# Performance work log

Measured on AMD Instinct MI355X. Metric: run time of the kernel, lower is better.

The kernel has to match this reference:

```python
import jax, jax.numpy as jnp
import numpy as np

N = 100000
E = 3200000
FEAT_DIMS = [512, 256, 128]
NUM_GNN = 2
NUM_MLP = 2
EPS = 1e-12


def l2norm(x):
    # F.normalize(x, dim=1, p=2)
    n = jnp.sqrt(jnp.sum(x * x, axis=1, keepdims=True))
    return x / jnp.maximum(n, EPS)


def setup_inputs() -> dict:
    key = jax.random.key(0)
    ks = jax.random.split(key, 16)
    D = FEAT_DIMS[-1]
    inp = {
        "feat": jax.random.normal(ks[0], (N, FEAT_DIMS[0]), dtype=jnp.float32),
        "sup_rows": jax.random.randint(ks[1], (E,), 0, N, dtype=jnp.int32),
        "sup_cols": jax.random.randint(ks[2], (E,), 0, N, dtype=jnp.int32),
        "sup_vals": jax.random.uniform(ks[3], (E,), dtype=jnp.float32),
        # feature-reduction linears (stored [in, out])
        "W_feat0": jax.random.normal(ks[4], (FEAT_DIMS[0], FEAT_DIMS[1]), dtype=jnp.float32) * 0.05,
        "b_feat0": jnp.zeros((FEAT_DIMS[1],), dtype=jnp.float32),
        "W_feat1": jax.random.normal(ks[5], (FEAT_DIMS[1], FEAT_DIMS[2]), dtype=jnp.float32) * 0.05,
        "b_feat1": jnp.zeros((FEAT_DIMS[2],), dtype=jnp.float32),
        # GCN layers (bias=False)
        "W_gnn": jax.random.normal(ks[6], (NUM_GNN, D, D), dtype=jnp.float32) * 0.05,
        # final emb linear map
        "W_emb": jax.random.normal(ks[7], (D, D), dtype=jnp.float32) * 0.05,
        "b_emb": jnp.zeros((D,), dtype=jnp.float32),
        # temperature MLP towers
        "W_lft": jax.random.normal(ks[8], (NUM_MLP, D, D), dtype=jnp.float32) * 0.05,
        "b_lft": jnp.zeros((NUM_MLP, D), dtype=jnp.float32),
        "W_rgt": jax.random.normal(ks[9], (NUM_MLP, D, D), dtype=jnp.float32) * 0.05,
        "b_rgt": jnp.zeros((NUM_MLP, D), dtype=jnp.float32),
    }
    return inp


def _forward(feat, sup_rows, sup_cols, sup_vals,
             W_feat0, b_feat0, W_feat1, b_feat1,
             W_gnn, W_emb, b_emb, W_lft, b_lft, W_rgt, b_rgt):
    # non-linear feature reduction (dropout = identity in eval mode)
    x = jnp.tanh(feat @ W_feat0 + b_feat0)
    x = jnp.tanh(x @ W_feat1 + b_feat1)

    def spmm(emb):
        # sparse support @ emb via gather + segment-sum
        msgs = sup_vals[:, None] * emb[sup_cols]           # [E, D]
        return jax.ops.segment_sum(msgs, sup_rows, num_segments=N)

    gnn_in = x
    gnn_acc = x
    gnn_out = x
    for l in range(NUM_GNN):
        h = spmm(gnn_in)
        h = jnp.tanh(h @ W_gnn[l])
        gnn_out = l2norm(h)
        gnn_in = gnn_out
        gnn_acc = gnn_acc + gnn_out

    emb = l2norm(gnn_acc @ W_emb + b_emb)

    lft_in = gnn_out
    rgt_in = gnn_out
    for l in range(NUM_MLP):
        lft = jnp.tanh(lft_in @ W_lft[l] + b_lft[l])
        rgt = jnp.tanh(rgt_in @ W_rgt[l] + b_rgt[l])
        if l < NUM_MLP - 1:
            lft = lft + lft_in
            rgt = rgt + rgt_in
        lft_in, rgt_in = lft, rgt
    return emb, lft_in, rgt_in


def reference(feat, sup_rows, sup_cols, sup_vals,
              W_feat0, b_feat0, W_feat1, b_feat1,
              W_gnn, W_emb, b_emb, W_lft, b_lft, W_rgt, b_rgt):
    return _forward(feat, sup_rows, sup_cols, sup_vals,
                    W_feat0, b_feat0, W_feat1, b_feat1,
                    W_gnn, W_emb, b_emb, W_lft, b_lft, W_rgt, b_rgt)
```

## Files before the change

kernel.cpp:

```cpp
#include <hip/hip_runtime.h>
#include <math.h>

typedef short bf16x8 __attribute__((ext_vector_type(8)));
typedef float f32x4  __attribute__((ext_vector_type(4)));

__device__ __forceinline__ unsigned short f2bf(float x) {
    unsigned u = __float_as_uint(x);
    unsigned r = u + 0x7FFFu + ((u >> 16) & 1u);
    return (unsigned short)(r >> 16);
}
__device__ __forceinline__ float bf2f(unsigned short b) {
    return __uint_as_float(((unsigned)b) << 16);
}

__global__ __launch_bounds__(256)
void wconvD(const float* __restrict__ W, unsigned short* __restrict__ Wt, int K, int N)
{
    int id = blockIdx.x * 256 + threadIdx.x;
    if (id >= K * N) return;
    int c = id / K, k = id - c * K;
    int kblk = k >> 5, ksub = (k >> 3) & 3, kel = k & 7;
    int cblk = c >> 6, n = c & 3, lr = (c >> 2) & 15;
    int lane = lr + (ksub << 4);
    size_t dst = ((((size_t)kblk * (N >> 6) + cblk) * 4 + n) << 9) + (lane << 3) + kel;
    Wt[dst] = f2bf(W[(size_t)k * N + c]);
}

__global__ __launch_bounds__(256)
void wconv7(const float* __restrict__ Wg, const float* __restrict__ Wemb,
            const float* __restrict__ Wl, const float* __restrict__ Wr,
            unsigned short* __restrict__ dst)
{
    int id = blockIdx.x * 256 + threadIdx.x;
    if (id >= 7 * 16384) return;
    int m = id >> 14, r = id & 16383;
    int c = r >> 7, k = r & 127;
    const float* src = (m < 2) ? (Wg + m * 16384)
                     : (m == 2) ? Wemb
                     : (m < 5) ? (Wl + (m - 3) * 16384)
                               : (Wr + (m - 5) * 16384);
    int n = c & 7, lr = (c >> 3) & 15;
    int ks = k >> 5, ksub = (k >> 3) & 3, kel = k & 7;
    int lane = lr + (ksub << 4);
    dst[(size_t)m * 16384 + (((ks << 3) + n) << 9) + (lane << 3) + kel] = f2bf(src[(size_t)k * 128 + c]);
}

__global__ __launch_bounds__(256)
void f32_to_bf16(const float* __restrict__ in, unsigned short* __restrict__ outb, long n8)
{
    long id = (long)blockIdx.x * 256 + threadIdx.x;
    if (id >= n8) return;
    const float4* p = (const float4*)(in + id * 8);
    float4 a = p[0], b = p[1];
    *(ushort4*)(outb + id * 8)     = make_ushort4(f2bf(a.x), f2bf(a.y), f2bf(a.z), f2bf(a.w));
    *(ushort4*)(outb + id * 8 + 4) = make_ushort4(f2bf(b.x), f2bf(b.y), f2bf(b.z), f2bf(b.w));
}

__global__ __launch_bounds__(256)
void mfma_direct(const unsigned short* __restrict__ Ab, const unsigned short* __restrict__ Wt,
                 const float* __restrict__ bias, unsigned short* __restrict__ out_bf,
                 int M, int K, int Ncols)
{
    const int tid  = threadIdx.x;
    const int row0 = blockIdx.x * 128;
    const int col0 = blockIdx.y * 128;
    const int wv   = tid >> 6, lane = tid & 63;
    const int wr   = (wv >> 1) * 64, wc = (wv & 1) * 64;
    const int lr   = lane & 15;
    const int lk8  = (lane >> 4) * 8;
    const int ncb  = Ncols >> 6;
    const int cp   = (col0 + wc) >> 6;

    const unsigned short* arow[4];
#pragma unroll
    for (int m = 0; m < 4; m++) {
        int r = row0 + wr + m * 16 + lr;
        r = r < M ? r : (M - 1);
        arow[m] = Ab + (size_t)r * K + lk8;
    }
    const unsigned short* bb = Wt + (((size_t)cp * 4) << 9) + (lane << 3);
    const size_t bstep = (size_t)ncb * 2048;

    f32x4 acc[4][4];
#pragma unroll
    for (int m = 0; m < 4; m++)
#pragma unroll
        for (int n = 0; n < 4; n++)
#pragma unroll
            for (int j = 0; j < 4; j++) acc[m][n][j] = 0.f;

#pragma unroll 2
    for (int kk = 0; kk < K; kk += 32) {
        bf16x8 af[4], bfr[4];
#pragma unroll
        for (int m = 0; m < 4; m++) af[m]  = *(const bf16x8*)(arow[m] + kk);
        const unsigned short* bk = bb + (size_t)(kk >> 5) * bstep;
#pragma unroll
        for (int n = 0; n < 4; n++) bfr[n] = *(const bf16x8*)(bk + (n << 9));
#pragma unroll
        for (int m = 0; m < 4; m++)
#pragma unroll
            for (int n = 0; n < 4; n++)
                acc[m][n] = __builtin_amdgcn_mfma_f32_16x16x32_bf16(af[m], bfr[n], acc[m][n], 0, 0, 0);
    }

    const int cbase = col0 + wc + lr * 4;
    float4 b4 = *(const float4*)(bias + cbase);
    float bv[4] = {b4.x, b4.y, b4.z, b4.w};
    const int rbase = (lane >> 4) * 4;
#pragma unroll
    for (int m = 0; m < 4; m++) {
#pragma unroll
        for (int j = 0; j < 4; j++) {
            int row = row0 + wr + m * 16 + rbase + j;
            if (row < M) {
                ushort4 o;
                o.x = f2bf(tanhf(acc[m][0][j] + bv[0]));
                o.y = f2bf(tanhf(acc[m][1][j] + bv[1]));
                o.z = f2bf(tanhf(acc[m][2][j] + bv[2]));
                o.w = f2bf(tanhf(acc[m][3][j] + bv[3]));
                *(ushort4*)(out_bf + (size_t)row * Ncols + cbase) = o;
            }
        }
    }
}

template<bool ABF16, bool TANH, bool L2, bool RESID, bool AUX, bool AUXBF,
         bool F32OUT, bool BF16OUT, bool BIAS>
__global__ __launch_bounds__(256)
void mfma_ep(const void* __restrict__ A_, const unsigned short* __restrict__ Wt,
             const float* __restrict__ bias, const unsigned short* __restrict__ resid_bf,
             const void* __restrict__ aux_in, float* __restrict__ aux_out,
             float* __restrict__ out, unsigned short* __restrict__ out_bf, int M)
{
    const int tid  = threadIdx.x;
    const int row0 = blockIdx.x * 64;
    const int wv   = tid >> 6, lane = tid & 63;
    const int lr   = lane & 15;
    const int lk8  = (lane >> 4) * 8;
    const int wr   = wv * 16;

    const unsigned short* Abr;
    const float*          Afr;
    {
        int r = row0 + wr + lr;
        r = r < M ? r : (M - 1);
        Abr = (const unsigned short*)A_ + ((size_t)r << 7) + lk8;
        Afr = (const float*)A_          + ((size_t)r << 7) + lk8;
    }
    const unsigned short* wb = Wt + (lane << 3);

    f32x4 acc[8];
#pragma unroll
    for (int n = 0; n < 8; n++)
#pragma unroll
        for (int j = 0; j < 4; j++) acc[n][j] = 0.f;

#pragma unroll 2
    for (int ks = 0; ks < 4; ks++) {
        bf16x8 af, bn[8];
        if (ABF16) af = *(const bf16x8*)(Abr + ks * 32);
        else {
            float4 a = *(const float4*)(Afr + ks * 32);
            float4 b = *(const float4*)(Afr + ks * 32 + 4);
            af[0]=(short)f2bf(a.x); af[1]=(short)f2bf(a.y); af[2]=(short)f2bf(a.z); af[3]=(short)f2bf(a.w);
            af[4]=(short)f2bf(b.x); af[5]=(short)f2bf(b.y); af[6]=(short)f2bf(b.z); af[7]=(short)f2bf(b.w);
        }
#pragma unroll
        for (int n = 0; n < 8; n++)
            bn[n] = *(const bf16x8*)(wb + ((((ks << 3) + n)) << 9));
#pragma unroll
        for (int n = 0; n < 8; n++)
            acc[n] = __builtin_amdgcn_mfma_f32_16x16x32_bf16(af, bn[n], acc[n], 0, 0, 0);
    }

    const int cbase = lr * 8;
    float bv[8];
    if (BIAS) {
        float4 b0 = *(const float4*)(bias + cbase);
        float4 b1 = *(const float4*)(bias + cbase + 4);
        bv[0]=b0.x; bv[1]=b0.y; bv[2]=b0.z; bv[3]=b0.w;
        bv[4]=b1.x; bv[5]=b1.y; bv[6]=b1.z; bv[7]=b1.w;
    } else {
#pragma unroll
        for (int n = 0; n < 8; n++) bv[n] = 0.f;
    }
    const int rbase = (lane >> 4) * 4;

#pragma unroll
    for (int j = 0; j < 4; j++) {
        int row = row0 + wr + rbase + j;
        bool ok = row < M;
        size_t base = ((size_t)row << 7) + cbase;
        float v[8];
#pragma unroll
        for (int n = 0; n < 8; n++) {
            v[n] = acc[n][j] + bv[n];
            if (TANH) v[n] = tanhf(v[n]);
        }
        if (RESID) {
            if (ok) {
                bf16x8 rv = *(const bf16x8*)(resid_bf + base);
#pragma unroll
                for (int n = 0; n < 8; n++) v[n] += bf2f((unsigned short)rv[n]);
            }
        }
        if (L2) {
            float s = 0.f;
#pragma unroll
            for (int n = 0; n < 8; n++) s += v[n] * v[n];
#pragma unroll
            for (int msk = 8; msk >= 1; msk >>= 1) s += __shfl_xor(s, msk);
            float sc = 1.f / fmaxf(sqrtf(s), 1e-12f);
#pragma unroll
            for (int n = 0; n < 8; n++) v[n] *= sc;
        }
        if (ok) {
            if (F32OUT) {
                *(float4*)(out + base)     = make_float4(v[0], v[1], v[2], v[3]);
                *(float4*)(out + base + 4) = make_float4(v[4], v[5], v[6], v[7]);
            }
            if (BF16OUT) {
                bf16x8 o;
#pragma unroll
                for (int n = 0; n < 8; n++) o[n] = (short)f2bf(v[n]);
                *(bf16x8*)(out_bf + base) = o;
            }
            if (AUX) {
                float ai[8];
                if (AUXBF) {
                    bf16x8 av = *(const bf16x8*)((const unsigned short*)aux_in + base);
#pragma unroll
                    for (int n = 0; n < 8; n++) ai[n] = bf2f((unsigned short)av[n]);
                } else {
                    float4 a0 = *(const float4*)((const float*)aux_in + base);
                    float4 a1 = *(const float4*)((const float*)aux_in + base + 4);
                    ai[0]=a0.x; ai[1]=a0.y; ai[2]=a0.z; ai[3]=a0.w;
                    ai[4]=a1.x; ai[5]=a1.y; ai[6]=a1.z; ai[7]=a1.w;
                }
                *(float4*)(aux_out + base)     = make_float4(ai[0]+v[0], ai[1]+v[1], ai[2]+v[2], ai[3]+v[3]);
                *(float4*)(aux_out + base + 4) = make_float4(ai[4]+v[4], ai[5]+v[5], ai[6]+v[6], ai[7]+v[7]);
            }
        }
    }
}

__global__ __launch_bounds__(256)
void tail_fused(const unsigned short* __restrict__ h_bf, const float* __restrict__ accf,
                const unsigned short* __restrict__ Wt7,
                const float* __restrict__ bemb, const float* __restrict__ bl,
                const float* __restrict__ br,
                float* __restrict__ embO, float* __restrict__ lftO,
                float* __restrict__ rgtO, int M)
{
    __shared__ __align__(16) unsigned short ldsA[4][16][136];
    __shared__ __align__(16) unsigned short ldsB[4][16][136];

    const int tid = threadIdx.x;
    const int wv = tid >> 6, lane = tid & 63;
    const int lr = lane & 15;
    const int lk8 = (lane >> 4) * 8;
    const int rbase = (lane >> 4) * 4;
    const int row0 = blockIdx.x * 64 + wv * 16;
    const int cbase = lr * 8;

    const unsigned short* Wg1t  = Wt7 + 1 * 16384 + (lane << 3);
    const unsigned short* Wembt = Wt7 + 2 * 16384 + (lane << 3);
    const unsigned short* Wl0t  = Wt7 + 3 * 16384 + (lane << 3);
    const unsigned short* Wl1t  = Wt7 + 4 * 16384 + (lane << 3);
    const unsigned short* Wr0t  = Wt7 + 5 * 16384 + (lane << 3);
    const unsigned short* Wr1t  = Wt7 + 6 * 16384 + (lane << 3);

    f32x4 acc[8];

#define ZACC() { _Pragma("unroll") for (int n = 0; n < 8; n++) \
                 _Pragma("unroll") for (int q = 0; q < 4; q++) acc[n][q] = 0.f; }
#define MM128(AFRAG, WPTR)                                                            \
    _Pragma("unroll")                                                                 \
    for (int ks = 0; ks < 4; ks++) {                                                  \
        bf16x8 af = (AFRAG);                                                          \
        bf16x8 bn[8];                                                                 \
        _Pragma("unroll")                                                             \
        for (int n = 0; n < 8; n++)                                                   \
            bn[n] = *(const bf16x8*)((WPTR) + ((((ks << 3) + n)) << 9));              \
        _Pragma("unroll")                                                             \
        for (int n = 0; n < 8; n++)                                                   \
            acc[n] = __builtin_amdgcn_mfma_f32_16x16x32_bf16(af, bn[n], acc[n], 0, 0, 0); \
    }
#define LDBIAS(BV, P) { float4 b0_ = *(const float4*)((P) + cbase);                   \
                        float4 b1_ = *(const float4*)((P) + cbase + 4);               \
                        BV[0]=b0_.x; BV[1]=b0_.y; BV[2]=b0_.z; BV[3]=b0_.w;           \
                        BV[4]=b1_.x; BV[5]=b1_.y; BV[6]=b1_.z; BV[7]=b1_.w; }
#define L2NORM(V) { float s_ = 0.f;                                                   \
                    _Pragma("unroll") for (int n = 0; n < 8; n++) s_ += V[n]*V[n];    \
                    _Pragma("unroll") for (int mk = 8; mk >= 1; mk >>= 1) s_ += __shfl_xor(s_, mk); \
                    float sc_ = 1.f / fmaxf(sqrtf(s_), 1e-12f);                       \
                    _Pragma("unroll") for (int n = 0; n < 8; n++) V[n] *= sc_; }

    const unsigned short* hrow;
    {
        int r = row0 + lr;
        r = r < M ? r : (M - 1);
        hrow = h_bf + ((size_t)r << 7) + lk8;
    }
    ZACC();
    MM128(*(const bf16x8*)(hrow + ks * 32), Wg1t);
#pragma unroll
    for (int j = 0; j < 4; j++) {
        int row = row0 + rbase + j;
        int rc = row < M ? row : (M - 1);
        float v[8];
#pragma unroll
        for (int n = 0; n < 8; n++) v[n] = tanhf(acc[n][j]);
        L2NORM(v);
        bf16x8 o;
#pragma unroll
        for (int n = 0; n < 8; n++) o[n] = (short)f2bf(v[n]);
        *(bf16x8*)&ldsA[wv][rbase + j][cbase] = o;
        float4 a0 = *(const float4*)(accf + ((size_t)rc << 7) + cbase);
        float4 a1 = *(const float4*)(accf + ((size_t)rc << 7) + cbase + 4);
        float av[8] = {a0.x+v[0], a0.y+v[1], a0.z+v[2], a0.w+v[3],
                       a1.x+v[4], a1.y+v[5], a1.z+v[6], a1.w+v[7]};
        bf16x8 ob;
#pragma unroll
        for (int n = 0; n < 8; n++) ob[n] = (short)f2bf(av[n]);
        *(bf16x8*)&ldsB[wv][rbase + j][cbase] = ob;
    }

    ZACC();
    MM128(*(const bf16x8*)&ldsB[wv][lr][ks * 32 + lk8], Wembt);
    {
        float bv[8]; LDBIAS(bv, bemb);
#pragma unroll
        for (int j = 0; j < 4; j++) {
            int row = row0 + rbase + j;
            float v[8];
#pragma unroll
            for (int n = 0; n < 8; n++) v[n] = acc[n][j] + bv[n];
            L2NORM(v);
            if (row < M) {
                size_t base = ((size_t)row << 7) + cbase;
                *(float4*)(embO + base)     = make_float4(v[0], v[1], v[2], v[3]);
                *(float4*)(embO + base + 4) = make_float4(v[4], v[5], v[6], v[7]);
            }
        }
    }

    ZACC();
    MM128(*(const bf16x8*)&ldsA[wv][lr][ks * 32 + lk8], Wl0t);
    {
        float bv[8]; LDBIAS(bv, bl);
#pragma unroll
        for (int j = 0; j < 4; j++) {
            bf16x8 rv = *(const bf16x8*)&ldsA[wv][rbase + j][cbase];
            bf16x8 ob;
#pragma unroll
            for (int n = 0; n < 8; n++)
                ob[n] = (short)f2bf(tanhf(acc[n][j] + bv[n]) + bf2f((unsigned short)rv[n]));
            *(bf16x8*)&ldsB[wv][rbase + j][cbase] = ob;
        }
    }

    ZACC();
    MM128(*(const bf16x8*)&ldsB[wv][lr][ks * 32 + lk8], Wl1t);
    {
        float bv[8]; LDBIAS(bv, bl + 128);
#pragma unroll
        for (int j = 0; j < 4; j++) {
            int row = row0 + rbase + j;
            if (row < M) {
                size_t base = ((size_t)row << 7) + cbase;
                *(float4*)(lftO + base)     = make_float4(tanhf(acc[0][j]+bv[0]), tanhf(acc[1][j]+bv[1]),
                                                          tanhf(acc[2][j]+bv[2]), tanhf(acc[3][j]+bv[3]));
                *(float4*)(lftO + base + 4) = make_float4(tanhf(acc[4][j]+bv[4]), tanhf(acc[5][j]+bv[5]),
                                                          tanhf(acc[6][j]+bv[6]), tanhf(acc[7][j]+bv[7]));
            }
        }
    }

    ZACC();
    MM128(*(const bf16x8*)&ldsA[wv][lr][ks * 32 + lk8], Wr0t);
    {
        float bv[8]; LDBIAS(bv, br);
#pragma unroll
        for (int j = 0; j < 4; j++) {
            bf16x8 rv = *(const bf16x8*)&ldsA[wv][rbase + j][cbase];
            bf16x8 ob;
#pragma unroll
            for (int n = 0; n < 8; n++)
                ob[n] = (short)f2bf(tanhf(acc[n][j] + bv[n]) + bf2f((unsigned short)rv[n]));
            *(bf16x8*)&ldsB[wv][rbase + j][cbase] = ob;
        }
    }

    ZACC();
    MM128(*(const bf16x8*)&ldsB[wv][lr][ks * 32 + lk8], Wr1t);
    {
        float bv[8]; LDBIAS(bv, br + 128);
#pragma unroll
        for (int j = 0; j < 4; j++) {
            int row = row0 + rbase + j;
            if (row < M) {
                size_t base = ((size_t)row << 7) + cbase;
                *(float4*)(rgtO + base)     = make_float4(tanhf(acc[0][j]+bv[0]), tanhf(acc[1][j]+bv[1]),
                                                          tanhf(acc[2][j]+bv[2]), tanhf(acc[3][j]+bv[3]));
                *(float4*)(rgtO + base + 4) = make_float4(tanhf(acc[4][j]+bv[4]), tanhf(acc[5][j]+bv[5]),
                                                          tanhf(acc[6][j]+bv[6]), tanhf(acc[7][j]+bv[7]));
            }
        }
    }
#undef ZACC
#undef MM128
#undef LDBIAS
#undef L2NORM
}

#define RCHUNK 16384

__global__ __launch_bounds__(256)
void bhist_k(const int* __restrict__ rows, int* __restrict__ bcnt, int E, int NB)
{
    __shared__ int lc[1024];
    for (int b = threadIdx.x; b < NB; b += 256) lc[b] = 0;
    __syncthreads();
    int start = blockIdx.x * RCHUNK;
    int end = min(start + RCHUNK, E);
    for (int i = start + threadIdx.x; i < end; i += 256)
        atomicAdd(&lc[rows[i] >> 7], 1);
    __syncthreads();
    for (int b = threadIdx.x; b < NB; b += 256)
        if (lc[b]) atomicAdd(&bcnt[b], lc[b]);
}

__global__ __launch_bounds__(256)
void bucket_scan(const int* __restrict__ bcnt, int* __restrict__ bbase,
                 int* __restrict__ bcur, int NB)
{
    __shared__ int sdata[256];
    const int tid = threadIdx.x;
    int loc[4]; int s = 0;
#pragma unroll
    for (int j = 0; j < 4; j++) {
        int i = tid * 4 + j;
        int v = (i < NB) ? bcnt[i] : 0;
        loc[j] = s; s += v;
    }
    sdata[tid] = s;
    __syncthreads();
    int x = s;
    for (int off = 1; off < 256; off <<= 1) {
        int t = 0;
        if (tid >= off) t = sdata[tid - off];
        __syncthreads();
        x += t;
        sdata[tid] = x;
        __syncthreads();
    }
    int excl = x - s;
#pragma unroll
    for (int j = 0; j < 4; j++) {
        int i = tid * 4 + j;
        if (i < NB) { bbase[i] = excl + loc[j]; bcur[i] = excl + loc[j]; }
    }
    if (tid == 255) bbase[NB] = x;
}

__global__ __launch_bounds__(256)
void bucket_scatter(const int* __restrict__ rows, const int* __restrict__ cols,
                    const float* __restrict__ vals, int* __restrict__ bcur,
                    int2* __restrict__ tmp, int E, int NB)
{
    __shared__ int lcnt[1024];
    __shared__ int lbase[1024];
    for (int b = threadIdx.x; b < NB; b += 256) lcnt[b] = 0;
    __syncthreads();
    int start = blockIdx.x * RCHUNK;
    int end = min(start + RCHUNK, E);
    for (int i = start + threadIdx.x; i < end; i += 256)
        atomicAdd(&lcnt[rows[i] >> 7], 1);
    __syncthreads();
    for (int b = threadIdx.x; b < NB; b += 256) {
        int c = lcnt[b];
        lbase[b] = c ? atomicAdd(&bcur[b], c) : 0;
        lcnt[b] = 0;
    }
    __syncthreads();
    for (int i = start + threadIdx.x; i < end; i += 256) {
        int r = rows[i];
        int b = r >> 7;
        int off = atomicAdd(&lcnt[b], 1);
        tmp[lbase[b] + off] = make_int2(cols[i] | ((r & 127) << 17), __float_as_int(vals[i]));
    }
}

__global__ __launch_bounds__(256)
void csr_place(const int2* __restrict__ tmp, const int* __restrict__ bbase,
               int* __restrict__ rowptr, int2* __restrict__ packed, int M, int NB)
{
    __shared__ int lcnt[128];
    __shared__ int lofs[128];
    const int tid = threadIdx.x;
    const int b = blockIdx.x;
    const int s = bbase[b], e = bbase[b + 1];
    const int rb = b << 7;
    if (tid < 128) lcnt[tid] = 0;
    __syncthreads();
    for (int i = s + tid; i < e; i += 256)
        atomicAdd(&lcnt[(((unsigned)tmp[i].x) >> 17) & 127], 1);
    __syncthreads();
    if (tid == 0) {
        int run = s;
#pragma unroll 8
        for (int r = 0; r < 128; r++) { lofs[r] = run; run += lcnt[r]; }
    }
    __syncthreads();
    if (tid < 128 && rb + tid < M) rowptr[rb + tid] = lofs[tid];
    if (b == NB - 1 && tid == 0) rowptr[M] = e;
    if (tid < 128) lcnt[tid] = 0;
    __syncthreads();
    for (int i = s + tid; i < e; i += 256) {
        int2 t = tmp[i];
        int rl = (((unsigned)t.x) >> 17) & 127;
        int pos = lofs[rl] + atomicAdd(&lcnt[rl], 1);
        packed[pos] = make_int2(t.x & 0x1FFFF, t.y);
    }
}

__global__ __launch_bounds__(256)
void spmm_csr(const int* __restrict__ rowptr, const int2* __restrict__ packed,
              const unsigned short* __restrict__ embb, unsigned short* __restrict__ hb, int N)
{
    const int wv = threadIdx.x >> 6, lane = threadIdx.x & 63;
    const int g = lane >> 4, q = lane & 15;
    const int r = blockIdx.x * 4 + wv;
    if (r >= N) return;
    const int s = rowptr[r], e = rowptr[r + 1];
    const unsigned short* __restrict__ eb = embb + q * 8;

    float a0=0.f,a1=0.f,a2=0.f,a3=0.f,a4=0.f,a5=0.f,a6=0.f,a7=0.f;
    int i = s + g;
    for (; i + 12 < e; i += 16) {
#pragma unroll
        for (int u = 0; u < 4; u++) {
            int2 p = packed[i + 4 * u];
            uint4 m = *(const uint4*)(eb + ((size_t)p.x << 7));
            float v = __int_as_float(p.y);
            a0 += v * __uint_as_float(m.x << 16);
            a1 += v * __uint_as_float(m.x & 0xffff0000u);
            a2 += v * __uint_as_float(m.y << 16);
            a3 += v * __uint_as_float(m.y & 0xffff0000u);
            a4 += v * __uint_as_float(m.z << 16);
            a5 += v * __uint_as_float(m.z & 0xffff0000u);
            a6 += v * __uint_as_float(m.w << 16);
            a7 += v * __uint_as_float(m.w & 0xffff0000u);
        }
    }
    for (; i < e; i += 4) {
        int2 p = packed[i];
        uint4 m = *(const uint4*)(eb + ((size_t)p.x << 7));
        float v = __int_as_float(p.y);
        a0 += v * __uint_as_float(m.x << 16);
        a1 += v * __uint_as_float(m.x & 0xffff0000u);
        a2 += v * __uint_as_float(m.y << 16);
        a3 += v * __uint_as_float(m.y & 0xffff0000u);
        a4 += v * __uint_as_float(m.z << 16);
        a5 += v * __uint_as_float(m.z & 0xffff0000u);
        a6 += v * __uint_as_float(m.w << 16);
        a7 += v * __uint_as_float(m.w & 0xffff0000u);
    }
#pragma unroll
    for (int msk = 16; msk <= 32; msk <<= 1) {
        a0 += __shfl_xor(a0, msk); a1 += __shfl_xor(a1, msk);
        a2 += __shfl_xor(a2, msk); a3 += __shfl_xor(a3, msk);
        a4 += __shfl_xor(a4, msk); a5 += __shfl_xor(a5, msk);
        a6 += __shfl_xor(a6, msk); a7 += __shfl_xor(a7, msk);
    }
    if (g == 0) {
        unsigned o0 = (unsigned)f2bf(a0) | ((unsigned)f2bf(a1) << 16);
        unsigned o1 = (unsigned)f2bf(a2) | ((unsigned)f2bf(a3) << 16);
        unsigned o2 = (unsigned)f2bf(a4) | ((unsigned)f2bf(a5) << 16);
        unsigned o3 = (unsigned)f2bf(a6) | ((unsigned)f2bf(a7) << 16);
        *(uint4*)(hb + ((size_t)r << 7) + q * 8) = make_uint4(o0, o1, o2, o3);
    }
}

extern "C" void kernel_launch(void* const* d_in, const int* in_sizes, int n_in,
                              void* d_out, int out_size, void* d_ws, size_t ws_size,
                              hipStream_t stream)
{
    const float* feat  = (const float*)d_in[0];
    const int*   srows = (const int*)  d_in[1];
    const int*   scols = (const int*)  d_in[2];
    const float* svals = (const float*)d_in[3];
    const float* Wf0   = (const float*)d_in[4];
    const float* bf0   = (const float*)d_in[5];
    const float* Wf1   = (const float*)d_in[6];
    const float* bf1   = (const float*)d_in[7];
    const float* Wg    = (const float*)d_in[8];
    const float* Wemb  = (const float*)d_in[9];
    const float* bemb  = (const float*)d_in[10];
    const float* Wl    = (const float*)d_in[11];
    const float* bl    = (const float*)d_in[12];
    const float* Wr    = (const float*)d_in[13];
    const float* br    = (const float*)d_in[14];

    const int M = in_sizes[0] / 512;
    const int E = in_sizes[1];
    const int NB = (M + 127) >> 7;

    float* out = (float*)d_out;
    float* R0 = out;
    float* R1 = out + (size_t)M * 128;
    float* R2 = out + (size_t)M * 256;

    float* ws = (float*)d_ws;
    float* accf = ws;
    int2*  tmp  = (int2*)ws;
    int*   ip = (int*)(ws + (size_t)M * 128);
    int*   rowptr  = ip;
    int2*  packed  = (int2*)(ip + (((size_t)M + 4) & ~(size_t)3));
    int*   bcnt    = (int*)(packed + E);
    int*   bbase   = bcnt + 1024;
    int*   bcur    = bbase + 1032;
    unsigned short* h_ws = (unsigned short*)(bcur + 1024);
    unsigned short* Wt0  = h_ws + (size_t)M * 128;
    unsigned short* Wt1  = Wt0 + 256 * 512;
    unsigned short* Wt7  = Wt1 + 128 * 256;

    unsigned short* R0a = (unsigned short*)R0;
    unsigned short* R1a = (unsigned short*)R1;
    unsigned short* feat_bf = (unsigned short*)R0;
    unsigned short* x1_bf   = (unsigned short*)R2;
    unsigned short* x_bf    = R0a;
    unsigned short* n0_bf   = R1a;

    dim3 blk(256);
    const int gm128 = (M + 127) / 128;
    const int gm64  = (M + 63) / 64;
    const int nch   = (E + RCHUNK - 1) / RCHUNK;

    wconvD<<<(512*256 + 255)/256, blk, 0, stream>>>(Wf0, Wt0, 512, 256);
    wconvD<<<(256*128 + 255)/256, blk, 0, stream>>>(Wf1, Wt1, 256, 128);
    wconv7<<<(7*16384 + 255)/256, blk, 0, stream>>>(Wg, Wemb, Wl, Wr, Wt7);

    f32_to_bf16<<<(int)(((long)M * 64 + 255) / 256), blk, 0, stream>>>(feat, feat_bf, (long)M * 64);

    hipMemsetAsync(bcnt, 0, (size_t)NB * 4, stream);
    bhist_k<<<nch, blk, 0, stream>>>(srows, bcnt, E, NB);
    bucket_scan<<<1, blk, 0, stream>>>(bcnt, bbase, bcur, NB);
    bucket_scatter<<<nch, blk, 0, stream>>>(srows, scols, svals, bcur, tmp, E, NB);
    csr_place<<<NB, blk, 0, stream>>>(tmp, bbase, rowptr, packed, M, NB);

    mfma_direct<<<dim3(gm128,2),blk,0,stream>>>(feat_bf, Wt0, bf0, x1_bf, M, 512, 256);
    mfma_direct<<<dim3(gm128,1),blk,0,stream>>>(x1_bf, Wt1, bf1, x_bf, M, 256, 128);
    spmm_csr<<<(M + 3) / 4, blk, 0, stream>>>(rowptr, packed, x_bf, h_ws, M);
    mfma_ep<true,true,true,false,true,true,false,true,false><<<gm64,blk,0,stream>>>(
        h_ws, Wt7 , nullptr, nullptr, x_bf, accf, nullptr, n0_bf, M);
    spmm_csr<<<(M + 3) / 4, blk, 0, stream>>>(rowptr, packed, n0_bf, h_ws, M);
    tail_fused<<<gm64, blk, 0, stream>>>(h_ws, accf, Wt7, bemb, bl, br, R0, R1, R2, M);
}
```

Before: 727.6 us.

## Fuse the two feature-reduction GEMMs into one kernel through shared memory

Replaces the two mfma_direct launches with one 512-thread kernel. Each block computes a 64-row tile of tanh(feat@W0+b0), keeps the 256-wide bf16 intermediate in LDS, then multiplies it by W1 to produce x directly. This removes the global write and re-read of the 100000x256 intermediate and one launch. In exchange, each block reloads W0 from global/L2 for fewer rows, so weight traffic per row goes up, and the smaller tile may reduce MFMA reuse.

```diff
diff --git a/kernel.cpp b/kernel.cpp
--- a/kernel.cpp
+++ b/kernel.cpp
@@ -56,71 +56,93 @@
     *(ushort4*)(outb + id * 8 + 4) = make_ushort4(f2bf(b.x), f2bf(b.y), f2bf(b.z), f2bf(b.w));
 }
 
-__global__ __launch_bounds__(256)
-void mfma_direct(const unsigned short* __restrict__ Ab, const unsigned short* __restrict__ Wt,
-                 const float* __restrict__ bias, unsigned short* __restrict__ out_bf,
-                 int M, int K, int Ncols)
-{
+__global__ __launch_bounds__(512)
+void mfma_head(const unsigned short* __restrict__ Ab, const unsigned short* __restrict__ Wt0,
+               const float* __restrict__ bf0, const unsigned short* __restrict__ Wt1,
+               const float* __restrict__ bf1, unsigned short* __restrict__ x_bf, int M)
+{
+    __shared__ __align__(16) unsigned short x1s[4][16][264];
+
     const int tid  = threadIdx.x;
-    const int row0 = blockIdx.x * 128;
-    const int col0 = blockIdx.y * 128;
     const int wv   = tid >> 6, lane = tid & 63;
-    const int wr   = (wv >> 1) * 64, wc = (wv & 1) * 64;
+    const int rg   = wv >> 1, ch = wv & 1;
     const int lr   = lane & 15;
     const int lk8  = (lane >> 4) * 8;
-    const int ncb  = Ncols >> 6;
-    const int cp   = (col0 + wc) >> 6;
-
-    const unsigned short* arow[4];
-#pragma unroll
-    for (int m = 0; m < 4; m++) {
-        int r = row0 + wr + m * 16 + lr;
-        r = r < M ? r : (M - 1);
-        arow[m] = Ab + (size_t)r * K + lk8;
-    }
-    const unsigned short* bb = Wt + (((size_t)cp * 4) << 9) + (lane << 3);
-    const size_t bstep = (size_t)ncb * 2048;
-
-    f32x4 acc[4][4];
-#pragma unroll
-    for (int m = 0; m < 4; m++)
+    const int rbase = (lane >> 4) * 4;
+    const int row0 = blockIdx.x * 64 + rg * 16;
+
+    const unsigned short* arow;
+    { int r = row0 + lr; r = r < M ? r : (M - 1); arow = Ab + (size_t)r * 512 + lk8; }
+    const unsigned short* bb0 = Wt0 + ((((size_t)ch * 2) * 4) << 9) + (lane << 3);
+
+    f32x4 acc1[8];
+#pragma unroll
+    for (int s = 0; s < 8; s++)
+#pragma unroll
+        for (int q = 0; q < 4; q++) acc1[s][q] = 0.f;
+
+#pragma unroll 2
+    for (int kb = 0; kb < 16; kb++) {
+        bf16x8 af = *(const bf16x8*)(arow + kb * 32);
+        bf16x8 bn[8];
+        const unsigned short* bk = bb0 + (((size_t)kb * 16) << 9);
+#pragma unroll
+        for (int s = 0; s < 8; s++) bn[s] = *(const bf16x8*)(bk + ((size_t)s << 9));
+#pragma unroll
+        for (int s = 0; s < 8; s++)
+            acc1[s] = __builtin_amdgcn_mfma_f32_16x16x32_bf16(af, bn[s], acc1[s], 0, 0, 0);
+    }
+
+#pragma unroll
+    for (int cb = 0; cb < 2; cb++) {
+        int colp = (ch * 2 + cb) * 64 + lr * 4;
+        float4 b4 = *(const float4*)(bf0 + colp);
+        float bv[4] = {b4.x, b4.y, b4.z, b4.w};
+#pragma unroll
+        for (int j = 0; j < 4; j++) {
+            ushort4 o;
+            o.x = f2bf(tanhf(acc1[cb * 4 + 0][j] + bv[0]));
+            o.y = f2bf(tanhf(acc1[cb * 4 + 1][j] + bv[1]));
+            o.z = f2bf(tanhf(acc1[cb * 4 + 2][j] + bv[2]));
+            o.w = f2bf(tanhf(acc1[cb * 4 + 3][j] + bv[3]));
+            *(ushort4*)&x1s[rg][rbase + j][colp] = o;
+        }
+    }
+    __syncthreads();
+
+    const unsigned short* bb1 = Wt1 + ((((size_t)ch) * 4) << 9) + (lane << 3);
+
+    f32x4 acc2[4];
+#pragma unroll
+    for (int n = 0; n < 4; n++)
+#pragma unroll
+        for (int q = 0; q < 4; q++) acc2[n][q] = 0.f;
+
+#pragma unroll 2
+    for (int ks = 0; ks < 8; ks++) {
+        bf16x8 af = *(const bf16x8*)&x1s[rg][lr][ks * 32 + lk8];
+        bf16x8 bn[4];
+        const unsigned short* bk = bb1 + (((size_t)ks * 8) << 9);
+#pragma unroll
+        for (int n = 0; n < 4; n++) bn[n] = *(const bf16x8*)(bk + ((size_t)n << 9));
 #pragma unroll
         for (int n = 0; n < 4; n++)
-#pragma unroll
-            for (int j = 0; j < 4; j++) acc[m][n][j] = 0.f;
-
-#pragma unroll 2
-    for (int kk = 0; kk < K; kk += 32) {
-        bf16x8 af[4], bfr[4];
-#pragma unroll
-        for (int m = 0; m < 4; m++) af[m]  = *(const bf16x8*)(arow[m] + kk);
-        const unsigned short* bk = bb + (size_t)(kk >> 5) * bstep;
-#pragma unroll
-        for (int n = 0; n < 4; n++) bfr[n] = *(const bf16x8*)(bk + (n << 9));
-#pragma unroll
-        for (int m = 0; m < 4; m++)
-#pragma unroll
-            for (int n = 0; n < 4; n++)
-                acc[m][n] = __builtin_amdgcn_mfma_f32_16x16x32_bf16(af[m], bfr[n], acc[m][n], 0, 0, 0);
-    }
-
-    const int cbase = col0 + wc + lr * 4;
-    float4 b4 = *(const float4*)(bias + cbase);
+            acc2[n] = __builtin_amdgcn_mfma_f32_16x16x32_bf16(af, bn[n], acc2[n], 0, 0, 0);
+    }
+
+    const int cbase = ch * 64 + lr * 4;
+    float4 b4 = *(const float4*)(bf1 + cbase);
     float bv[4] = {b4.x, b4.y, b4.z, b4.w};
-    const int rbase = (lane >> 4) * 4;
-#pragma unroll
-    for (int m = 0; m < 4; m++) {
-#pragma unroll
-        for (int j = 0; j < 4; j++) {
-            int row = row0 + wr + m * 16 + rbase + j;
-            if (row < M) {
-                ushort4 o;
-                o.x = f2bf(tanhf(acc[m][0][j] + bv[0]));
-                o.y = f2bf(tanhf(acc[m][1][j] + bv[1]));
-                o.z = f2bf(tanhf(acc[m][2][j] + bv[2]));
-                o.w = f2bf(tanhf(acc[m][3][j] + bv[3]));
-                *(ushort4*)(out_bf + (size_t)row * Ncols + cbase) = o;
-            }
+#pragma unroll
+    for (int j = 0; j < 4; j++) {
+        int row = row0 + rbase + j;
+        if (row < M) {
+            ushort4 o;
+            o.x = f2bf(tanhf(acc2[0][j] + bv[0]));
+            o.y = f2bf(tanhf(acc2[1][j] + bv[1]));
+            o.z = f2bf(tanhf(acc2[2][j] + bv[2]));
+            o.w = f2bf(tanhf(acc2[3][j] + bv[3]));
+            *(ushort4*)(x_bf + ((size_t)row << 7) + cbase) = o;
         }
     }
 }
@@ -630,14 +652,12 @@
     unsigned short* R0a = (unsigned short*)R0;
     unsigned short* R1a = (unsigned short*)R1;
     unsigned short* feat_bf = (unsigned short*)R0;
-    unsigned short* x1_bf   = (unsigned short*)R2;
-    unsigned short* x_bf    = R0a;
+    unsigned short* x_bf    = (unsigned short*)R2;
     unsigned short* n0_bf   = R1a;
 
     dim3 blk(256);
-    const int gm128 = (M + 127) / 128;
-    const int gm64  = (M + 63) / 64;
-    const int nch   = (E + RCHUNK - 1) / RCHUNK;
+    const int gm64 = (M + 63) / 64;
+    const int nch  = (E + RCHUNK - 1) / RCHUNK;
 
     wconvD<<<(512*256 + 255)/256, blk, 0, stream>>>(Wf0, Wt0, 512, 256);
     wconvD<<<(256*128 + 255)/256, blk, 0, stream>>>(Wf1, Wt1, 256, 128);
@@ -651,8 +671,7 @@
     bucket_scatter<<<nch, blk, 0, stream>>>(srows, scols, svals, bcur, tmp, E, NB);
     csr_place<<<NB, blk, 0, stream>>>(tmp, bbase, rowptr, packed, M, NB);
 
-    mfma_direct<<<dim3(gm128,2),blk,0,stream>>>(feat_bf, Wt0, bf0, x1_bf, M, 512, 256);
-    mfma_direct<<<dim3(gm128,1),blk,0,stream>>>(x1_bf, Wt1, bf1, x_bf, M, 256, 128);
+    mfma_head<<<gm64, dim3(512), 0, stream>>>(feat_bf, Wt0, bf0, Wt1, bf1, x_bf, M);
     spmm_csr<<<(M + 3) / 4, blk, 0, stream>>>(rowptr, packed, x_bf, h_ws, M);
     mfma_ep<true,true,true,false,true,true,false,true,false><<<gm64,blk,0,stream>>>(
         h_ws, Wt7 , nullptr, nullptr, x_bf, accf, nullptr, n0_bf, M);
```

Result: no change. 729.6 us (+0.3%).
